# Kernel tuning notes

Hardware: AMD Instinct MI355X
Metric: run time of the kernel (lower is better)

The kernel has to match this reference:

```python
import jax, jax.numpy as jnp
import numpy as np

KS = 3          # kernel_size
NK = KS * KS    # sample points per output pixel
PAD = KS // 2   # 'same' zero padding


def setup_inputs() -> dict:
    key = jax.random.key(0)
    k1, k2, k3, k4 = jax.random.split(key, 4)
    B, H, W, C, F = 8, 64, 64, 128, 256
    x = jax.random.normal(k1, (B, H, W, C), jnp.float32)
    offset = jax.random.normal(k2, (B, H, W, 2 * NK), jnp.float32)
    modulation = jax.random.uniform(k3, (B, H, W, NK), jnp.float32)
    conv_kernel = jax.random.normal(k4, (KS, KS, C, F), jnp.float32) * 0.02
    conv_bias = jnp.zeros((F,), jnp.float32)
    return {"x": x, "offset": offset, "modulation": modulation,
            "conv_kernel": conv_kernel, "conv_bias": conv_bias}


def reference(x, offset, modulation, conv_kernel, conv_bias):
    B, H, W, C = x.shape
    # zero pad ('same')
    xp = jnp.pad(x, ((0, 0), (PAD, PAD), (PAD, PAD), (0, 0)))
    ih, iw = H + 2 * PAD, W + 2 * PAD

    # offset: first NK channels are y-offsets, last NK are x-offsets -> [B,H,W,NK,2]
    off = jnp.stack([offset[..., :NK], offset[..., NK:]], axis=-1)

    # pixel centers in padded coords (start at 1 due to padding), stride 1
    gy, gx = jnp.meshgrid(jnp.arange(1, H + 1), jnp.arange(1, W + 1), indexing="ij")
    pix = jnp.stack([gy, gx], -1).reshape(1, H, W, 1, 2).astype(x.dtype)

    # kernel tap offsets, ky varies slowest after flatten (matches TF source)
    ky, kx = jnp.meshgrid(jnp.arange(-PAD, KS - PAD), jnp.arange(-PAD, KS - PAD), indexing="ij")
    ker = jnp.stack([ky.reshape(-1), kx.reshape(-1)], -1).reshape(1, 1, 1, NK, 2).astype(x.dtype)

    p = off + pix + ker                       # [B,H,W,NK,2] sampling locations
    y0f = jnp.floor(p[..., 0])
    x0f = jnp.floor(p[..., 1])
    y0 = jnp.clip(y0f, 0, ih - 1)
    x0 = jnp.clip(x0f, 0, iw - 1)
    y1 = jnp.clip(y0f + 1.0, 0, ih - 1)
    x1 = jnp.clip(x0f + 1.0, 0, iw - 1)

    bidx = jnp.arange(B).reshape(B, 1, 1, 1)

    def gather(yi, xi):  # -> [B,H,W,NK,C]
        return xp[bidx, yi.astype(jnp.int32), xi.astype(jnp.int32)]

    f00 = gather(y0, x0)
    f01 = gather(y1, x0)
    f10 = gather(y0, x1)
    f11 = gather(y1, x1)

    py = jnp.clip(p[..., 0], 0, ih - 1)[..., None]
    px = jnp.clip(p[..., 1], 0, iw - 1)[..., None]
    ly = py - y0[..., None]
    lx = px - x0[..., None]

    feats = ((1.0 - ly) * (1.0 - lx) * f00 + (1.0 - ly) * lx * f01
             + ly * (1.0 - lx) * f10 + ly * lx * f11)      # [B,H,W,NK,C]
    feats = feats * modulation[..., None]

    # rearrange exactly as the TF code: concat kernel-row chunks along H, then reshape
    feats = jnp.concatenate([feats[:, :, :, s:s + KS, :] for s in range(0, NK, KS)], axis=1)
    feats = feats.reshape(B, H * KS, W * KS, C)

    out = jax.lax.conv_general_dilated(
        feats, conv_kernel, window_strides=(KS, KS), padding="VALID",
        dimension_numbers=("NHWC", "HWIO", "NHWC"))
    return out + conv_bias
```

## Files before the change

kernel.cpp:

```cpp
#include <hip/hip_runtime.h>

typedef __attribute__((ext_vector_type(8))) short short8;
typedef __attribute__((ext_vector_type(4))) float f32x4;

__device__ __forceinline__ unsigned short f2bf(float f) {
  union { float f; unsigned u; } v; v.f = f;
  unsigned r = v.u + 0x7FFFu + ((v.u >> 16) & 1u);
  return (unsigned short)(r >> 16);
}

__device__ __forceinline__ short8 pack8(f32x4 a, f32x4 b) {
  short8 p;
  p[0] = (short)f2bf(a.x); p[1] = (short)f2bf(a.y);
  p[2] = (short)f2bf(a.z); p[3] = (short)f2bf(a.w);
  p[4] = (short)f2bf(b.x); p[5] = (short)f2bf(b.y);
  p[6] = (short)f2bf(b.z); p[7] = (short)f2bf(b.w);
  return p;
}

__device__ __forceinline__ short8 packEO(f32x4 e, f32x4 o) {
  short8 p;
  p[0] = (short)f2bf(e.x); p[1] = (short)f2bf(o.x);
  p[2] = (short)f2bf(e.y); p[3] = (short)f2bf(o.y);
  p[4] = (short)f2bf(e.z); p[5] = (short)f2bf(o.z);
  p[6] = (short)f2bf(e.w); p[7] = (short)f2bf(o.w);
  return p;
}

constexpr int KKt = 1152;
constexpr int Ff  = 256;
constexpr size_t WT_BYTES = (size_t)KKt * Ff * 2;
constexpr size_t XB_BYTES = (size_t)8 * 64 * 64 * 128 * 2;

__global__ void wt_prep(const float* __restrict__ kf, unsigned short* __restrict__ wtB) {
  int idx = blockIdx.x * 256 + threadIdx.x;
  int j  = idx & 7;
  int fr = (idx >> 3) & 15;
  int kg = (idx >> 7) & 3;
  int ft = (idx >> 9) & 15;
  int ks = (idx >> 13) & 3;
  int ch = idx >> 15;
  int k = ch * 128 + ks * 32 + kg * 8 + j;
  int f = ft * 16 + fr;
  wtB[idx] = f2bf(kf[k * Ff + f]);
}

__global__ void x_prep(const float* __restrict__ x, unsigned short* __restrict__ xb) {
  int i = (blockIdx.x * 512 + threadIdx.x) * 8;
  const f32x4* p = (const f32x4*)(x + i);
  *(short8*)(xb + i) = pack8(p[0], p[1]);
}

__global__ __launch_bounds__(1024, 8) void dcn_bf16(
    const unsigned short* __restrict__ xb, const float* __restrict__ off,
    const float* __restrict__ mo, const unsigned short* __restrict__ wtB,
    const float* __restrict__ bias, float* __restrict__ out) {
  __shared__ __align__(16) char At[2][64 * 272];

  const int b  = blockIdx.x & 7;
  const int oh = blockIdx.x >> 3;
  const int t  = threadIdx.x;
  const int lane = t & 63;
  const int wv   = t >> 6;
  const int mh   = wv & 1;
  const int fq   = wv >> 1;
  const int fr   = lane & 15;
  const int kg   = lane >> 4;
  const int sow  = t >> 4;
  const int c8   = t & 15;

  f32x4 acc[2][2];
#pragma unroll
  for (int i = 0; i < 2; ++i) { acc[i][0] = f32x4{0,0,0,0}; acc[i][1] = f32x4{0,0,0,0}; }

  float oyr[2], oxr[2], mmr[2];
  int   og[4]; float wg[4];

  auto loadOff = [&](int ch, int sl) {
    const int dy = ch / 3, dxk = ch - dy * 3;
    const int r = 3 * oh + dy, hp = r & 63, kp = ((r >> 6) * 3) + dxk;
    const int pix = (b * 64 + hp) * 64 + sow;
    oyr[sl] = off[pix * 18 + kp];
    oxr[sl] = off[pix * 18 + 9 + kp];
    mmr[sl] = mo[pix * 9 + kp];
  };

  auto calcW = [&](int ch, int sl) {
    const int dy = ch / 3, dxk = ch - dy * 3;
    const int r = 3 * oh + dy, hp = r & 63, kp = ((r >> 6) * 3) + dxk;
    const float py = oyr[sl] + (float)(hp + kp / 3);
    const float px = oxr[sl] + (float)(sow + kp % 3);
    const float mm = mmr[sl];
    const float y0f = floorf(py), x0f = floorf(px);
    const float y0 = fminf(fmaxf(y0f, 0.f), 65.f);
    const float y1 = fminf(fmaxf(y0f + 1.f, 0.f), 65.f);
    const float x0 = fminf(fmaxf(x0f, 0.f), 65.f);
    const float x1 = fminf(fmaxf(x0f + 1.f, 0.f), 65.f);
    const float ly = fminf(fmaxf(py, 0.f), 65.f) - y0;
    const float lx = fminf(fmaxf(px, 0.f), 65.f) - x0;
    wg[0] = (1.f - ly) * (1.f - lx) * mm;
    wg[1] = (1.f - ly) * lx * mm;
    wg[2] = ly * (1.f - lx) * mm;
    wg[3] = ly * lx * mm;
    const int iy0 = (int)y0, iy1 = (int)y1, ix0 = (int)x0, ix1 = (int)x1;
    const int yy[4] = {iy0, iy1, iy0, iy1};
    const int xx[4] = {ix0, ix0, ix1, ix1};
#pragma unroll
    for (int j = 0; j < 4; ++j) {
      const bool v = (yy[j] >= 1) & (yy[j] <= 64) & (xx[j] >= 1) & (xx[j] <= 64);
      int o = ((b * 64 + yy[j] - 1) * 64 + (xx[j] - 1)) * 128 + c8 * 8;
      if (!v) { o = 0; wg[j] = 0.f; }
      og[j] = o;
    }
  };

  auto ldQ = [&](int c) -> short8 {
    return *(const short8*)(xb + og[c]);
  };
  auto accQ = [&](short8 s, float w, f32x4& Pe, f32x4& Po) {
    union { short8 s; unsigned u[4]; } v; v.s = s;
#pragma unroll
    for (int i = 0; i < 4; ++i) {
      union { unsigned u; float f; } e, o;
      e.u = v.u[i] << 16;
      o.u = v.u[i] & 0xffff0000u;
      Pe[i] = fmaf(w, e.f, Pe[i]);
      Po[i] = fmaf(w, o.f, Po[i]);
    }
  };

  auto mmah = [&](int buf, int ch, int ks) {
    const unsigned short* bp = wtB + (((ch * 4 + ks) * 16 + fq * 2) * 64 + lane) * 8;
    short8 bf0 = *(const short8*)bp;
    short8 bf1 = *(const short8*)(bp + 512);
    short8 af[2];
#pragma unroll
    for (int m2 = 0; m2 < 2; ++m2)
      af[m2] = *(const short8*)(At[buf] + (mh * 32 + m2 * 16 + fr) * 272 + ks * 64 + kg * 16);
#pragma unroll
    for (int m2 = 0; m2 < 2; ++m2) {
      acc[m2][0] = __builtin_amdgcn_mfma_f32_16x16x32_bf16(af[m2], bf0, acc[m2][0], 0, 0, 0);
      acc[m2][1] = __builtin_amdgcn_mfma_f32_16x16x32_bf16(af[m2], bf1, acc[m2][1], 0, 0, 0);
    }
  };

  const int wb = sow * 272 + c8 * 16;

  loadOff(0, 0); loadOff(1, 1);
  calcW(0, 0);
  {
    short8 q0 = ldQ(0), q1 = ldQ(1), q2 = ldQ(2), q3 = ldQ(3);
    f32x4 Pe{0,0,0,0}, Po{0,0,0,0};
    accQ(q0, wg[0], Pe, Po); accQ(q1, wg[1], Pe, Po);
    accQ(q2, wg[2], Pe, Po); accQ(q3, wg[3], Pe, Po);
    *(short8*)(At[0] + wb) = packEO(Pe, Po);
  }
  __syncthreads();

#pragma unroll
  for (int ch = 0; ch < 9; ++ch) {
    const int buf = ch & 1;
    const bool hv = ch < 8;
    short8 q0, q1, q2, q3;
    f32x4 Pe{0,0,0,0}, Po{0,0,0,0};
    if (hv) {
      calcW(ch + 1, (ch + 1) & 1);
      q0 = ldQ(0); q1 = ldQ(1);
    }
    mmah(buf, ch, 0);
    if (hv) {
      q2 = ldQ(2); q3 = ldQ(3);
      accQ(q0, wg[0], Pe, Po);
    }
    mmah(buf, ch, 1);
    if (hv) accQ(q1, wg[1], Pe, Po);
    if (ch < 7) loadOff(ch + 2, ch & 1);
    mmah(buf, ch, 2);
    if (hv) {
      accQ(q2, wg[2], Pe, Po);
      accQ(q3, wg[3], Pe, Po);
      *(short8*)(At[buf ^ 1] + wb) = packEO(Pe, Po);
    }
    mmah(buf, ch, 3);
    __syncthreads();
  }

  float bs[2];
#pragma unroll
  for (int nb = 0; nb < 2; ++nb) bs[nb] = bias[fq * 32 + nb * 16 + fr];
  float* orow = out + (long)(b * 64 + oh) * 64 * 256;
#pragma unroll
  for (int m2 = 0; m2 < 2; ++m2) {
#pragma unroll
    for (int j = 0; j < 4; ++j) {
      const int row = mh * 32 + m2 * 16 + kg * 4 + j;
#pragma unroll
      for (int nb = 0; nb < 2; ++nb)
        orow[row * 256 + fq * 32 + nb * 16 + fr] = acc[m2][nb][j] + bs[nb];
    }
  }
}

__global__ __launch_bounds__(512, 4) void dcn_f32(
    const float* __restrict__ x, const float* __restrict__ off,
    const float* __restrict__ mo, const unsigned short* __restrict__ wtB,
    const float* __restrict__ bias, float* __restrict__ out) {
  __shared__ __align__(16) char At[2][64 * 272];
  const int b  = blockIdx.x & 7;
  const int oh = blockIdx.x >> 3;
  const int t  = threadIdx.x;
  const int lane = t & 63;
  const int wv   = t >> 6;
  const int fr   = lane & 15;
  const int kg   = lane >> 4;
  const int sow  = t >> 3;
  const int c16  = t & 7;

  f32x4 acc[4][2];
#pragma unroll
  for (int i = 0; i < 4; ++i) { acc[i][0] = f32x4{0,0,0,0}; acc[i][1] = f32x4{0,0,0,0}; }
  float oyr[2], oxr[2], mmr[2];
  int   og[4]; float wg[4];

  auto loadOff = [&](int ch, int sl) {
    const int dy = ch / 3, dxk = ch - dy * 3;
    const int r = 3 * oh + dy, hp = r & 63, kp = ((r >> 6) * 3) + dxk;
    const int pix = (b * 64 + hp) * 64 + sow;
    oyr[sl] = off[pix * 18 + kp];
    oxr[sl] = off[pix * 18 + 9 + kp];
    mmr[sl] = mo[pix * 9 + kp];
  };
  auto calcW = [&](int ch, int sl) {
    const int dy = ch / 3, dxk = ch - dy * 3;
    const int r = 3 * oh + dy, hp = r & 63, kp = ((r >> 6) * 3) + dxk;
    const float py = oyr[sl] + (float)(hp + kp / 3);
    const float px = oxr[sl] + (float)(sow + kp % 3);
    const float mm = mmr[sl];
    const float y0f = floorf(py), x0f = floorf(px);
    const float y0 = fminf(fmaxf(y0f, 0.f), 65.f);
    const float y1 = fminf(fmaxf(y0f + 1.f, 0.f), 65.f);
    const float x0 = fminf(fmaxf(x0f, 0.f), 65.f);
    const float x1 = fminf(fmaxf(x0f + 1.f, 0.f), 65.f);
    const float ly = fminf(fmaxf(py, 0.f), 65.f) - y0;
    const float lx = fminf(fmaxf(px, 0.f), 65.f) - x0;
    wg[0] = (1.f - ly) * (1.f - lx) * mm;
    wg[1] = (1.f - ly) * lx * mm;
    wg[2] = ly * (1.f - lx) * mm;
    wg[3] = ly * lx * mm;
    const int iy0 = (int)y0, iy1 = (int)y1, ix0 = (int)x0, ix1 = (int)x1;
    const int yy[4] = {iy0, iy1, iy0, iy1};
    const int xx[4] = {ix0, ix0, ix1, ix1};
#pragma unroll
    for (int j = 0; j < 4; ++j) {
      const bool v = (yy[j] >= 1) & (yy[j] <= 64) & (xx[j] >= 1) & (xx[j] <= 64);
      int o = ((b * 64 + yy[j] - 1) * 64 + (xx[j] - 1)) * 128 + c16 * 16;
      if (!v) { o = 0; wg[j] = 0.f; }
      og[j] = o;
    }
  };
  auto ldB = [&](int ch, int ks, short8* bf) {
    const unsigned short* p = wtB + (((ch * 4 + ks) * 16 + wv * 2) * 64 + lane) * 8;
    bf[0] = *(const short8*)p;
    bf[1] = *(const short8*)(p + 512);
  };
  auto mmah = [&](int buf, int ks, const short8* bf) {
    short8 af[4];
#pragma unroll
    for (int m2 = 0; m2 < 4; ++m2)
      af[m2] = *(const short8*)(At[buf] + (m2 * 16 + fr) * 272 + ks * 64 + kg * 16);
#pragma unroll
    for (int m2 = 0; m2 < 4; ++m2)
#pragma unroll
      for (int nb = 0; nb < 2; ++nb)
        acc[m2][nb] = __builtin_amdgcn_mfma_f32_16x16x32_bf16(af[m2], bf[nb], acc[m2][nb], 0, 0, 0);
  };
  auto ldC = [&](int c, f32x4* G) {
    const f32x4* p = (const f32x4*)(x + og[c]);
    G[0] = p[0]; G[1] = p[1]; G[2] = p[2]; G[3] = p[3];
  };
  const int wb = sow * 272 + c16 * 32;
  loadOff(0, 0); loadOff(1, 1);
  calcW(0, 0);
  {
    f32x4 G0[4], G1[4];
    ldC(0, G0); ldC(1, G1);
    f32x4 P0 = wg[0]*G0[0] + wg[1]*G1[0], P1 = wg[0]*G0[1] + wg[1]*G1[1];
    f32x4 P2 = wg[0]*G0[2] + wg[1]*G1[2], P3 = wg[0]*G0[3] + wg[1]*G1[3];
    ldC(2, G0); ldC(3, G1);
    P0 += wg[2]*G0[0] + wg[3]*G1[0]; P1 += wg[2]*G0[1] + wg[3]*G1[1];
    P2 += wg[2]*G0[2] + wg[3]*G1[2]; P3 += wg[2]*G0[3] + wg[3]*G1[3];
    *(short8*)(At[0] + wb)      = pack8(P0, P1);
    *(short8*)(At[0] + wb + 16) = pack8(P2, P3);
  }
  __syncthreads();
#pragma unroll
  for (int ch = 0; ch < 9; ++ch) {
    const int buf = ch & 1;
    const bool hv = ch < 8;
    if (hv) calcW(ch + 1, (ch + 1) & 1);
    short8 bA[2], bB[2];
    f32x4 G0[4], G1[4], P0, P1, P2, P3;
    ldB(ch, 0, bA);
    if (hv) ldC(0, G0);
    ldB(ch, 1, bB);
    mmah(buf, 0, bA);
    if (hv) { P0 = wg[0]*G0[0]; P1 = wg[0]*G0[1]; P2 = wg[0]*G0[2]; P3 = wg[0]*G0[3]; }
    if (hv) ldC(1, G1);
    ldB(ch, 2, bA);
    mmah(buf, 1, bB);
    if (hv) { P0 += wg[1]*G1[0]; P1 += wg[1]*G1[1]; P2 += wg[1]*G1[2]; P3 += wg[1]*G1[3]; }
    if (hv) ldC(2, G0);
    ldB(ch, 3, bB);
    if (ch < 7) loadOff(ch + 2, ch & 1);
    mmah(buf, 2, bA);
    if (hv) { P0 += wg[2]*G0[0]; P1 += wg[2]*G0[1]; P2 += wg[2]*G0[2]; P3 += wg[2]*G0[3]; }
    if (hv) ldC(3, G1);
    mmah(buf, 3, bB);
    if (hv) {
      P0 += wg[3]*G1[0]; P1 += wg[3]*G1[1]; P2 += wg[3]*G1[2]; P3 += wg[3]*G1[3];
      *(short8*)(At[buf ^ 1] + wb)      = pack8(P0, P1);
      *(short8*)(At[buf ^ 1] + wb + 16) = pack8(P2, P3);
    }
    __syncthreads();
  }
  float bs[2];
#pragma unroll
  for (int nb = 0; nb < 2; ++nb) bs[nb] = bias[wv * 32 + nb * 16 + fr];
  float* orow = out + (long)(b * 64 + oh) * 64 * 256;
#pragma unroll
  for (int m2 = 0; m2 < 4; ++m2) {
#pragma unroll
    for (int j = 0; j < 4; ++j) {
      const int ow = m2 * 16 + kg * 4 + j;
#pragma unroll
      for (int nb = 0; nb < 2; ++nb)
        orow[ow * 256 + wv * 32 + nb * 16 + fr] = acc[m2][nb][j] + bs[nb];
    }
  }
}

extern "C" void kernel_launch(void* const* d_in, const int* in_sizes, int n_in,
                              void* d_out, int out_size, void* d_ws, size_t ws_size,
                              hipStream_t stream) {
  const float* x    = (const float*)d_in[0];
  const float* off  = (const float*)d_in[1];
  const float* mo   = (const float*)d_in[2];
  const float* kf   = (const float*)d_in[3];
  const float* bias = (const float*)d_in[4];
  float* outp = (float*)d_out;
  unsigned short* wtB = (unsigned short*)d_ws;

  wt_prep<<<1152, 256, 0, stream>>>(kf, wtB);
  if (ws_size >= WT_BYTES + XB_BYTES) {
    unsigned short* xb = (unsigned short*)((char*)d_ws + WT_BYTES);
    x_prep<<<1024, 512, 0, stream>>>(x, xb);
    dcn_bf16<<<512, 1024, 0, stream>>>(xb, off, mo, wtB, bias, outp);
  } else {
    dcn_f32<<<512, 512, 0, stream>>>(x, off, mo, wtB, bias, outp);
  }
}
```

Baseline: 57.05 us.

## Precompute bilinear sample records in a fused prep kernel and simplify main loop

```diff
diff --git a/kernel.cpp b/kernel.cpp
--- a/kernel.cpp
+++ b/kernel.cpp
@@ -2,6 +2,7 @@
 
 typedef __attribute__((ext_vector_type(8))) short short8;
 typedef __attribute__((ext_vector_type(4))) float f32x4;
+typedef __attribute__((ext_vector_type(4))) int   int4v;
 
 __device__ __forceinline__ unsigned short f2bf(float f) {
   union { float f; unsigned u; } v; v.f = f;
@@ -29,8 +30,190 @@
 
 constexpr int KKt = 1152;
 constexpr int Ff  = 256;
-constexpr size_t WT_BYTES = (size_t)KKt * Ff * 2;
-constexpr size_t XB_BYTES = (size_t)8 * 64 * 64 * 128 * 2;
+constexpr size_t WT_BYTES  = (size_t)KKt * Ff * 2;
+constexpr size_t XB_BYTES  = (size_t)8 * 64 * 64 * 128 * 2;
+constexpr size_t REC_BYTES = (size_t)8 * 192 * 3 * 64 * 32;
+
+__global__ __launch_bounds__(256) void prep_all(
+    const float* __restrict__ x, const float* __restrict__ off,
+    const float* __restrict__ mo, const float* __restrict__ kf,
+    unsigned short* __restrict__ wtB, unsigned short* __restrict__ xb,
+    float* __restrict__ rec) {
+  const int bid = blockIdx.x;
+  if (bid < 2048) {
+    int i = (bid * 256 + threadIdx.x) * 8;
+    const f32x4* p = (const f32x4*)(x + i);
+    *(short8*)(xb + i) = pack8(p[0], p[1]);
+  } else if (bid < 2048 + 1152) {
+    int idx = (bid - 2048) * 256 + threadIdx.x;
+    int j  = idx & 7;
+    int fr = (idx >> 3) & 15;
+    int kg = (idx >> 7) & 3;
+    int ft = (idx >> 9) & 15;
+    int ks = (idx >> 13) & 3;
+    int ch = idx >> 15;
+    int k = ch * 128 + ks * 32 + kg * 8 + j;
+    int f = ft * 16 + fr;
+    wtB[idx] = f2bf(kf[k * Ff + f]);
+  } else {
+    int s  = (bid - 3200) * 256 + threadIdx.x;
+    int w  = s & 63;
+    int t1 = s >> 6;
+    int dxk = t1 % 3;
+    int t2  = t1 / 3;
+    int r   = t2 % 192;
+    int b   = t2 / 192;
+    int hp  = r & 63;
+    int kp  = (r >> 6) * 3 + dxk;
+    int pix = (b * 64 + hp) * 64 + w;
+    float oy = off[pix * 18 + kp];
+    float ox = off[pix * 18 + 9 + kp];
+    float mm = mo[pix * 9 + kp];
+    float py = oy + (float)(hp + kp / 3);
+    float px = ox + (float)(w + kp % 3);
+    float y0f = floorf(py), x0f = floorf(px);
+    float y0 = fminf(fmaxf(y0f, 0.f), 65.f);
+    float y1 = fminf(fmaxf(y0f + 1.f, 0.f), 65.f);
+    float x0 = fminf(fmaxf(x0f, 0.f), 65.f);
+    float x1 = fminf(fmaxf(x0f + 1.f, 0.f), 65.f);
+    float ly = fminf(fmaxf(py, 0.f), 65.f) - y0;
+    float lx = fminf(fmaxf(px, 0.f), 65.f) - x0;
+    f32x4 wv;
+    wv.x = (1.f - ly) * (1.f - lx) * mm;
+    wv.y = (1.f - ly) * lx * mm;
+    wv.z = ly * (1.f - lx) * mm;
+    wv.w = ly * lx * mm;
+    const int iy0 = (int)y0, iy1 = (int)y1, ix0 = (int)x0, ix1 = (int)x1;
+    const int yy[4] = {iy0, iy1, iy0, iy1};
+    const int xx[4] = {ix0, ix0, ix1, ix1};
+    int4v ov;
+#pragma unroll
+    for (int j2 = 0; j2 < 4; ++j2) {
+      const bool v = (yy[j2] >= 1) & (yy[j2] <= 64) & (xx[j2] >= 1) & (xx[j2] <= 64);
+      int o = ((b * 64 + yy[j2] - 1) * 64 + (xx[j2] - 1)) * 128;
+      if (!v) { o = 0; wv[j2] = 0.f; }
+      ov[j2] = o;
+    }
+    ((f32x4*)rec)[s * 2]     = wv;
+    ((int4v*)rec)[s * 2 + 1] = ov;
+  }
+}
+
+__global__ __launch_bounds__(1024, 8) void dcn_rec(
+    const unsigned short* __restrict__ xb, const unsigned short* __restrict__ wtB,
+    const float* __restrict__ rec, const float* __restrict__ bias,
+    float* __restrict__ out) {
+  __shared__ __align__(16) char At[2][64 * 272];
+
+  const int b  = blockIdx.x & 7;
+  const int oh = blockIdx.x >> 3;
+  const int t  = threadIdx.x;
+  const int lane = t & 63;
+  const int wv   = t >> 6;
+  const int mh   = wv & 1;
+  const int fq   = wv >> 1;
+  const int fr   = lane & 15;
+  const int kg   = lane >> 4;
+  const int sow  = t >> 4;
+  const int c8   = t & 15;
+
+  f32x4 acc[2][2];
+#pragma unroll
+  for (int i = 0; i < 2; ++i) { acc[i][0] = f32x4{0,0,0,0}; acc[i][1] = f32x4{0,0,0,0}; }
+
+  const f32x4* rp = (const f32x4*)rec + (size_t)((b * 576 + 9 * oh) * 64) * 2;
+
+  auto ldR = [&](int ch, f32x4& w4, int4v& o4) {
+    const f32x4* p = rp + (ch * 64 + sow) * 2;
+    w4 = p[0];
+    o4 = *(const int4v*)(p + 1);
+  };
+  auto issueG = [&](int4v o4, short8* q) {
+    q[0] = *(const short8*)(xb + o4.x + c8 * 8);
+    q[1] = *(const short8*)(xb + o4.y + c8 * 8);
+    q[2] = *(const short8*)(xb + o4.z + c8 * 8);
+    q[3] = *(const short8*)(xb + o4.w + c8 * 8);
+  };
+  auto accQ = [&](short8 s, float w, f32x4& Pe, f32x4& Po) {
+    union { short8 s; unsigned u[4]; } v; v.s = s;
+#pragma unroll
+    for (int i = 0; i < 4; ++i) {
+      union { unsigned u; float f; } e, o;
+      e.u = v.u[i] << 16;
+      o.u = v.u[i] & 0xffff0000u;
+      Pe[i] = fmaf(w, e.f, Pe[i]);
+      Po[i] = fmaf(w, o.f, Po[i]);
+    }
+  };
+  auto combine = [&](const short8* q, f32x4 w4) -> short8 {
+    f32x4 Pe{0,0,0,0}, Po{0,0,0,0};
+    accQ(q[0], w4.x, Pe, Po);
+    accQ(q[1], w4.y, Pe, Po);
+    accQ(q[2], w4.z, Pe, Po);
+    accQ(q[3], w4.w, Pe, Po);
+    return packEO(Pe, Po);
+  };
+  auto mmah = [&](int buf, int ch, int ks) {
+    const unsigned short* bp = wtB + (((ch * 4 + ks) * 16 + fq * 2) * 64 + lane) * 8;
+    short8 bf0 = *(const short8*)bp;
+    short8 bf1 = *(const short8*)(bp + 512);
+    short8 af[2];
+#pragma unroll
+    for (int m2 = 0; m2 < 2; ++m2)
+      af[m2] = *(const short8*)(At[buf] + (mh * 32 + m2 * 16 + fr) * 272 + ks * 64 + kg * 16);
+#pragma unroll
+    for (int m2 = 0; m2 < 2; ++m2) {
+      acc[m2][0] = __builtin_amdgcn_mfma_f32_16x16x32_bf16(af[m2], bf0, acc[m2][0], 0, 0, 0);
+      acc[m2][1] = __builtin_amdgcn_mfma_f32_16x16x32_bf16(af[m2], bf1, acc[m2][1], 0, 0, 0);
+    }
+  };
+
+  const int wb = sow * 272 + c8 * 16;
+
+  short8 q[4];
+  f32x4  w4s[2];
+  int4v  o4;
+
+  ldR(0, w4s[0], o4);
+  issueG(o4, q);
+  {
+    int4v o4b;
+    ldR(1, w4s[1], o4b);
+    *(short8*)(At[0] + wb) = combine(q, w4s[0]);
+    issueG(o4b, q);
+  }
+  __syncthreads();
+
+#pragma unroll
+  for (int ch = 0; ch < 9; ++ch) {
+    const int buf = ch & 1;
+    int4v o4n;
+    if (ch < 7) ldR(ch + 2, w4s[ch & 1], o4n);
+    if (ch < 8)
+      *(short8*)(At[buf ^ 1] + wb) = combine(q, w4s[(ch + 1) & 1]);
+    mmah(buf, ch, 0);
+    mmah(buf, ch, 1);
+    if (ch < 7) issueG(o4n, q);
+    mmah(buf, ch, 2);
+    mmah(buf, ch, 3);
+    __syncthreads();
+  }
+
+  float bs[2];
+#pragma unroll
+  for (int nb = 0; nb < 2; ++nb) bs[nb] = bias[fq * 32 + nb * 16 + fr];
+  float* orow = out + (long)(b * 64 + oh) * 64 * 256;
+#pragma unroll
+  for (int m2 = 0; m2 < 2; ++m2) {
+#pragma unroll
+    for (int j = 0; j < 4; ++j) {
+      const int row = mh * 32 + m2 * 16 + kg * 4 + j;
+#pragma unroll
+      for (int nb = 0; nb < 2; ++nb)
+        orow[row * 256 + fq * 32 + nb * 16 + fr] = acc[m2][nb][j] + bs[nb];
+    }
+  }
+}
 
 __global__ void wt_prep(const float* __restrict__ kf, unsigned short* __restrict__ wtB) {
   int idx = blockIdx.x * 256 + threadIdx.x;
@@ -56,7 +239,6 @@
     const float* __restrict__ mo, const unsigned short* __restrict__ wtB,
     const float* __restrict__ bias, float* __restrict__ out) {
   __shared__ __align__(16) char At[2][64 * 272];
-
   const int b  = blockIdx.x & 7;
   const int oh = blockIdx.x >> 3;
   const int t  = threadIdx.x;
@@ -72,7 +254,6 @@
   f32x4 acc[2][2];
 #pragma unroll
   for (int i = 0; i < 2; ++i) { acc[i][0] = f32x4{0,0,0,0}; acc[i][1] = f32x4{0,0,0,0}; }
-
   float oyr[2], oxr[2], mmr[2];
   int   og[4]; float wg[4];
 
@@ -84,7 +265,6 @@
     oxr[sl] = off[pix * 18 + 9 + kp];
     mmr[sl] = mo[pix * 9 + kp];
   };
-
   auto calcW = [&](int ch, int sl) {
     const int dy = ch / 3, dxk = ch - dy * 3;
     const int r = 3 * oh + dy, hp = r & 63, kp = ((r >> 6) * 3) + dxk;
@@ -113,10 +293,7 @@
       og[j] = o;
     }
   };
-
-  auto ldQ = [&](int c) -> short8 {
-    return *(const short8*)(xb + og[c]);
-  };
+  auto ldQ = [&](int c) -> short8 { return *(const short8*)(xb + og[c]); };
   auto accQ = [&](short8 s, float w, f32x4& Pe, f32x4& Po) {
     union { short8 s; unsigned u[4]; } v; v.s = s;
 #pragma unroll
@@ -128,7 +305,6 @@
       Po[i] = fmaf(w, o.f, Po[i]);
     }
   };
-
   auto mmah = [&](int buf, int ch, int ks) {
     const unsigned short* bp = wtB + (((ch * 4 + ks) * 16 + fq * 2) * 64 + lane) * 8;
     short8 bf0 = *(const short8*)bp;
@@ -143,9 +319,7 @@
       acc[m2][1] = __builtin_amdgcn_mfma_f32_16x16x32_bf16(af[m2], bf1, acc[m2][1], 0, 0, 0);
     }
   };
-
   const int wb = sow * 272 + c8 * 16;
-
   loadOff(0, 0); loadOff(1, 1);
   calcW(0, 0);
   {
@@ -156,7 +330,6 @@
     *(short8*)(At[0] + wb) = packEO(Pe, Po);
   }
   __syncthreads();
-
 #pragma unroll
   for (int ch = 0; ch < 9; ++ch) {
     const int buf = ch & 1;
@@ -184,7 +357,6 @@
     mmah(buf, ch, 3);
     __syncthreads();
   }
-
   float bs[2];
 #pragma unroll
   for (int nb = 0; nb < 2; ++nb) bs[nb] = bias[fq * 32 + nb * 16 + fr];
@@ -197,144 +369,6 @@
 #pragma unroll
       for (int nb = 0; nb < 2; ++nb)
         orow[row * 256 + fq * 32 + nb * 16 + fr] = acc[m2][nb][j] + bs[nb];
-    }
-  }
-}
-
-__global__ __launch_bounds__(512, 4) void dcn_f32(
-    const float* __restrict__ x, const float* __restrict__ off,
-    const float* __restrict__ mo, const unsigned short* __restrict__ wtB,
-    const float* __restrict__ bias, float* __restrict__ out) {
-  __shared__ __align__(16) char At[2][64 * 272];
-  const int b  = blockIdx.x & 7;
-  const int oh = blockIdx.x >> 3;
-  const int t  = threadIdx.x;
-  const int lane = t & 63;
-  const int wv   = t >> 6;
-  const int fr   = lane & 15;
-  const int kg   = lane >> 4;
-  const int sow  = t >> 3;
-  const int c16  = t & 7;
-
-  f32x4 acc[4][2];
-#pragma unroll
-  for (int i = 0; i < 4; ++i) { acc[i][0] = f32x4{0,0,0,0}; acc[i][1] = f32x4{0,0,0,0}; }
-  float oyr[2], oxr[2], mmr[2];
-  int   og[4]; float wg[4];
-
-  auto loadOff = [&](int ch, int sl) {
-    const int dy = ch / 3, dxk = ch - dy * 3;
-    const int r = 3 * oh + dy, hp = r & 63, kp = ((r >> 6) * 3) + dxk;
-    const int pix = (b * 64 + hp) * 64 + sow;
-    oyr[sl] = off[pix * 18 + kp];
-    oxr[sl] = off[pix * 18 + 9 + kp];
-    mmr[sl] = mo[pix * 9 + kp];
-  };
-  auto calcW = [&](int ch, int sl) {
-    const int dy = ch / 3, dxk = ch - dy * 3;
-    const int r = 3 * oh + dy, hp = r & 63, kp = ((r >> 6) * 3) + dxk;
-    const float py = oyr[sl] + (float)(hp + kp / 3);
-    const float px = oxr[sl] + (float)(sow + kp % 3);
-    const float mm = mmr[sl];
-    const float y0f = floorf(py), x0f = floorf(px);
-    const float y0 = fminf(fmaxf(y0f, 0.f), 65.f);
-    const float y1 = fminf(fmaxf(y0f + 1.f, 0.f), 65.f);
-    const float x0 = fminf(fmaxf(x0f, 0.f), 65.f);
-    const float x1 = fminf(fmaxf(x0f + 1.f, 0.f), 65.f);
-    const float ly = fminf(fmaxf(py, 0.f), 65.f) - y0;
-    const float lx = fminf(fmaxf(px, 0.f), 65.f) - x0;
-    wg[0] = (1.f - ly) * (1.f - lx) * mm;
-    wg[1] = (1.f - ly) * lx * mm;
-    wg[2] = ly * (1.f - lx) * mm;
-    wg[3] = ly * lx * mm;
-    const int iy0 = (int)y0, iy1 = (int)y1, ix0 = (int)x0, ix1 = (int)x1;
-    const int yy[4] = {iy0, iy1, iy0, iy1};
-    const int xx[4] = {ix0, ix0, ix1, ix1};
-#pragma unroll
-    for (int j = 0; j < 4; ++j) {
-      const bool v = (yy[j] >= 1) & (yy[j] <= 64) & (xx[j] >= 1) & (xx[j] <= 64);
-      int o = ((b * 64 + yy[j] - 1) * 64 + (xx[j] - 1)) * 128 + c16 * 16;
-      if (!v) { o = 0; wg[j] = 0.f; }
-      og[j] = o;
-    }
-  };
-  auto ldB = [&](int ch, int ks, short8* bf) {
-    const unsigned short* p = wtB + (((ch * 4 + ks) * 16 + wv * 2) * 64 + lane) * 8;
-    bf[0] = *(const short8*)p;
-    bf[1] = *(const short8*)(p + 512);
-  };
-  auto mmah = [&](int buf, int ks, const short8* bf) {
-    short8 af[4];
-#pragma unroll
-    for (int m2 = 0; m2 < 4; ++m2)
-      af[m2] = *(const short8*)(At[buf] + (m2 * 16 + fr) * 272 + ks * 64 + kg * 16);
-#pragma unroll
-    for (int m2 = 0; m2 < 4; ++m2)
-#pragma unroll
-      for (int nb = 0; nb < 2; ++nb)
-        acc[m2][nb] = __builtin_amdgcn_mfma_f32_16x16x32_bf16(af[m2], bf[nb], acc[m2][nb], 0, 0, 0);
-  };
-  auto ldC = [&](int c, f32x4* G) {
-    const f32x4* p = (const f32x4*)(x + og[c]);
-    G[0] = p[0]; G[1] = p[1]; G[2] = p[2]; G[3] = p[3];
-  };
-  const int wb = sow * 272 + c16 * 32;
-  loadOff(0, 0); loadOff(1, 1);
-  calcW(0, 0);
-  {
-    f32x4 G0[4], G1[4];
-    ldC(0, G0); ldC(1, G1);
-    f32x4 P0 = wg[0]*G0[0] + wg[1]*G1[0], P1 = wg[0]*G0[1] + wg[1]*G1[1];
-    f32x4 P2 = wg[0]*G0[2] + wg[1]*G1[2], P3 = wg[0]*G0[3] + wg[1]*G1[3];
-    ldC(2, G0); ldC(3, G1);
-    P0 += wg[2]*G0[0] + wg[3]*G1[0]; P1 += wg[2]*G0[1] + wg[3]*G1[1];
-    P2 += wg[2]*G0[2] + wg[3]*G1[2]; P3 += wg[2]*G0[3] + wg[3]*G1[3];
-    *(short8*)(At[0] + wb)      = pack8(P0, P1);
-    *(short8*)(At[0] + wb + 16) = pack8(P2, P3);
-  }
-  __syncthreads();
-#pragma unroll
-  for (int ch = 0; ch < 9; ++ch) {
-    const int buf = ch & 1;
-    const bool hv = ch < 8;
-    if (hv) calcW(ch + 1, (ch + 1) & 1);
-    short8 bA[2], bB[2];
-    f32x4 G0[4], G1[4], P0, P1, P2, P3;
-    ldB(ch, 0, bA);
-    if (hv) ldC(0, G0);
-    ldB(ch, 1, bB);
-    mmah(buf, 0, bA);
-    if (hv) { P0 = wg[0]*G0[0]; P1 = wg[0]*G0[1]; P2 = wg[0]*G0[2]; P3 = wg[0]*G0[3]; }
-    if (hv) ldC(1, G1);
-    ldB(ch, 2, bA);
-    mmah(buf, 1, bB);
-    if (hv) { P0 += wg[1]*G1[0]; P1 += wg[1]*G1[1]; P2 += wg[1]*G1[2]; P3 += wg[1]*G1[3]; }
-    if (hv) ldC(2, G0);
-    ldB(ch, 3, bB);
-    if (ch < 7) loadOff(ch + 2, ch & 1);
-    mmah(buf, 2, bA);
-    if (hv) { P0 += wg[2]*G0[0]; P1 += wg[2]*G0[1]; P2 += wg[2]*G0[2]; P3 += wg[2]*G0[3]; }
-    if (hv) ldC(3, G1);
-    mmah(buf, 3, bB);
-    if (hv) {
-      P0 += wg[3]*G1[0]; P1 += wg[3]*G1[1]; P2 += wg[3]*G1[2]; P3 += wg[3]*G1[3];
-      *(short8*)(At[buf ^ 1] + wb)      = pack8(P0, P1);
-      *(short8*)(At[buf ^ 1] + wb + 16) = pack8(P2, P3);
-    }
-    __syncthreads();
-  }
-  float bs[2];
-#pragma unroll
-  for (int nb = 0; nb < 2; ++nb) bs[nb] = bias[wv * 32 + nb * 16 + fr];
-  float* orow = out + (long)(b * 64 + oh) * 64 * 256;
-#pragma unroll
-  for (int m2 = 0; m2 < 4; ++m2) {
-#pragma unroll
-    for (int j = 0; j < 4; ++j) {
-      const int ow = m2 * 16 + kg * 4 + j;
-#pragma unroll
-      for (int nb = 0; nb < 2; ++nb)
-        orow[ow * 256 + wv * 32 + nb * 16 + fr] = acc[m2][nb][j] + bs[nb];
     }
   }
 }
@@ -349,13 +383,15 @@
   const float* bias = (const float*)d_in[4];
   float* outp = (float*)d_out;
   unsigned short* wtB = (unsigned short*)d_ws;
-
-  wt_prep<<<1152, 256, 0, stream>>>(kf, wtB);
-  if (ws_size >= WT_BYTES + XB_BYTES) {
-    unsigned short* xb = (unsigned short*)((char*)d_ws + WT_BYTES);
+  unsigned short* xb  = (unsigned short*)((char*)d_ws + WT_BYTES);
+
+  if (ws_size >= WT_BYTES + XB_BYTES + REC_BYTES) {
+    float* rec = (float*)((char*)d_ws + WT_BYTES + XB_BYTES);
+    prep_all<<<4352, 256, 0, stream>>>(x, off, mo, kf, wtB, xb, rec);
+    dcn_rec<<<512, 1024, 0, stream>>>(xb, wtB, rec, bias, outp);
+  } else {
+    wt_prep<<<1152, 256, 0, stream>>>(kf, wtB);
     x_prep<<<1024, 512, 0, stream>>>(x, xb);
     dcn_bf16<<<512, 1024, 0, stream>>>(xb, off, mo, wtB, bias, outp);
-  } else {
-    dcn_f32<<<512, 512, 0, stream>>>(x, off, mo, wtB, bias, outp);
-  }
-}
+  }
+}
```

Result: slower. 63.12 us (+10.6%).

## Split deformable sampling into a separate bf16 im2col pass and a pipelined GEMM

Applied to the files above, without the earlier changes.

```diff
diff --git a/kernel.cpp b/kernel.cpp
--- a/kernel.cpp
+++ b/kernel.cpp
@@ -31,24 +31,178 @@
 constexpr int Ff  = 256;
 constexpr size_t WT_BYTES = (size_t)KKt * Ff * 2;
 constexpr size_t XB_BYTES = (size_t)8 * 64 * 64 * 128 * 2;
-
-__global__ void wt_prep(const float* __restrict__ kf, unsigned short* __restrict__ wtB) {
-  int idx = blockIdx.x * 256 + threadIdx.x;
-  int j  = idx & 7;
-  int fr = (idx >> 3) & 15;
-  int kg = (idx >> 7) & 3;
-  int ft = (idx >> 9) & 15;
-  int ks = (idx >> 13) & 3;
-  int ch = idx >> 15;
-  int k = ch * 128 + ks * 32 + kg * 8 + j;
-  int f = ft * 16 + fr;
-  wtB[idx] = f2bf(kf[k * Ff + f]);
-}
-
-__global__ void x_prep(const float* __restrict__ x, unsigned short* __restrict__ xb) {
-  int i = (blockIdx.x * 512 + threadIdx.x) * 8;
-  const f32x4* p = (const f32x4*)(x + i);
-  *(short8*)(xb + i) = pack8(p[0], p[1]);
+constexpr size_t FE_BYTES = (size_t)32768 * KKt * 2;
+
+#define GLOAD_LDS16(g, l)                                          \
+  __builtin_amdgcn_global_load_lds(                                \
+      (const __attribute__((address_space(1))) void*)(g),          \
+      (__attribute__((address_space(3))) void*)(l), 16, 0, 0)
+
+__global__ __launch_bounds__(256) void prep_small(
+    const float* __restrict__ x, const float* __restrict__ kf,
+    unsigned short* __restrict__ xb, unsigned short* __restrict__ wtB) {
+  const int bid = blockIdx.x;
+  if (bid < 2048) {
+    int i = (bid * 256 + threadIdx.x) * 8;
+    const f32x4* p = (const f32x4*)(x + i);
+    *(short8*)(xb + i) = pack8(p[0], p[1]);
+  } else {
+    int idx = (bid - 2048) * 256 + threadIdx.x;
+    int j  = idx & 7;
+    int fr = (idx >> 3) & 15;
+    int kg = (idx >> 7) & 3;
+    int ft = (idx >> 9) & 15;
+    int ks = (idx >> 13) & 3;
+    int ch = idx >> 15;
+    int k = ch * 128 + ks * 32 + kg * 8 + j;
+    int f = ft * 16 + fr;
+    wtB[idx] = f2bf(kf[k * Ff + f]);
+  }
+}
+
+__global__ __launch_bounds__(1024, 8) void feats_prep(
+    const unsigned short* __restrict__ xb, const float* __restrict__ off,
+    const float* __restrict__ mo, char* __restrict__ feats) {
+  const int b  = blockIdx.x & 7;
+  const int oh = blockIdx.x >> 3;
+  const int t  = threadIdx.x;
+  const int sow = t >> 4;
+  const int c8  = t & 15;
+  const int r   = ((oh & 1) << 6) | sow;
+  const int mt  = (b << 5) | (oh >> 1);
+  const int swz = ((c8 & 7) << 4) ^ ((sow & 7) << 4);
+
+  for (int ch = 0; ch < 9; ++ch) {
+    const int dy = ch / 3, dxk = ch - dy * 3;
+    const int rr = 3 * oh + dy, hp = rr & 63, kp = ((rr >> 6) * 3) + dxk;
+    const int pix = (b * 64 + hp) * 64 + sow;
+    const float oy = off[pix * 18 + kp];
+    const float ox = off[pix * 18 + 9 + kp];
+    const float mm = mo[pix * 9 + kp];
+    const float py = oy + (float)(hp + kp / 3);
+    const float px = ox + (float)(sow + kp % 3);
+    const float y0f = floorf(py), x0f = floorf(px);
+    const float y0 = fminf(fmaxf(y0f, 0.f), 65.f);
+    const float y1 = fminf(fmaxf(y0f + 1.f, 0.f), 65.f);
+    const float x0 = fminf(fmaxf(x0f, 0.f), 65.f);
+    const float x1 = fminf(fmaxf(x0f + 1.f, 0.f), 65.f);
+    const float ly = fminf(fmaxf(py, 0.f), 65.f) - y0;
+    const float lx = fminf(fmaxf(px, 0.f), 65.f) - x0;
+    float wg[4];
+    wg[0] = (1.f - ly) * (1.f - lx) * mm;
+    wg[1] = (1.f - ly) * lx * mm;
+    wg[2] = ly * (1.f - lx) * mm;
+    wg[3] = ly * lx * mm;
+    const int iy0 = (int)y0, iy1 = (int)y1, ix0 = (int)x0, ix1 = (int)x1;
+    const int yy[4] = {iy0, iy1, iy0, iy1};
+    const int xx[4] = {ix0, ix0, ix1, ix1};
+    int og[4];
+#pragma unroll
+    for (int j = 0; j < 4; ++j) {
+      const bool v = (yy[j] >= 1) & (yy[j] <= 64) & (xx[j] >= 1) & (xx[j] <= 64);
+      int o = ((b * 64 + yy[j] - 1) * 64 + (xx[j] - 1)) * 128 + c8 * 8;
+      if (!v) { o = 0; wg[j] = 0.f; }
+      og[j] = o;
+    }
+    short8 q0 = *(const short8*)(xb + og[0]);
+    short8 q1 = *(const short8*)(xb + og[1]);
+    short8 q2 = *(const short8*)(xb + og[2]);
+    short8 q3 = *(const short8*)(xb + og[3]);
+    f32x4 Pe{0, 0, 0, 0}, Po{0, 0, 0, 0};
+    auto accQ = [&](short8 s, float w) {
+      union { short8 s; unsigned u[4]; } v; v.s = s;
+#pragma unroll
+      for (int i = 0; i < 4; ++i) {
+        union { unsigned u; float f; } e, o;
+        e.u = v.u[i] << 16;
+        o.u = v.u[i] & 0xffff0000u;
+        Pe[i] = fmaf(w, e.f, Pe[i]);
+        Po[i] = fmaf(w, o.f, Po[i]);
+      }
+    };
+    accQ(q0, wg[0]); accQ(q1, wg[1]); accQ(q2, wg[2]); accQ(q3, wg[3]);
+    const int kstep = ch * 2 + (c8 >> 3);
+    const size_t dst = ((size_t)(kstep * 256 + mt) << 14) + (size_t)r * 128 + swz;
+    *(short8*)(feats + dst) = packEO(Pe, Po);
+  }
+}
+
+__global__ __launch_bounds__(512, 4) void dcn_gemm(
+    const char* __restrict__ feats, const unsigned short* __restrict__ wtB,
+    const float* __restrict__ bias, float* __restrict__ out) {
+  __shared__ __align__(16) char As[2][16384];
+
+  const int bid = blockIdx.x;
+  const int b   = bid & 7;
+  const int q   = bid >> 3;
+  const int nt  = q & 1;
+  const int mt  = (b << 5) | (q >> 1);
+  const int t   = threadIdx.x;
+  const int lane = t & 63;
+  const int wv   = t >> 6;
+  const int wc   = wv & 3;
+  const int wr   = wv >> 2;
+  const int fr   = lane & 15;
+  const int kg   = lane >> 4;
+
+  f32x4 acc[4][2];
+#pragma unroll
+  for (int i = 0; i < 4; ++i) { acc[i][0] = f32x4{0,0,0,0}; acc[i][1] = f32x4{0,0,0,0}; }
+
+  const char* Abase = feats + ((size_t)mt << 14);
+  const int loff = (wv << 11) + (lane << 4);
+
+  auto stage = [&](int buf, int ks) {
+    const char* g = Abase + ((size_t)ks << 22);
+    GLOAD_LDS16(g + loff,        &As[buf][wv << 11]);
+    GLOAD_LDS16(g + loff + 1024, &As[buf][(wv << 11) + 1024]);
+  };
+
+  auto compute = [&](int buf, int ks) {
+#pragma unroll
+    for (int ks2 = 0; ks2 < 2; ++ks2) {
+      short8 af[4];
+#pragma unroll
+      for (int m2 = 0; m2 < 4; ++m2) {
+        const int rr = wr * 64 + m2 * 16 + fr;
+        af[m2] = *(const short8*)&As[buf][rr * 128 + ((ks2 * 64 + kg * 16) ^ ((rr & 7) << 4))];
+      }
+      const int ch = ks >> 1, ksB = ((ks & 1) << 1) | ks2;
+      const unsigned short* bp =
+          wtB + ((((ch * 4 + ksB) * 16 + nt * 8 + wc * 2) * 64 + lane) << 3);
+      short8 bf0 = *(const short8*)bp;
+      short8 bf1 = *(const short8*)(bp + 512);
+#pragma unroll
+      for (int m2 = 0; m2 < 4; ++m2) {
+        acc[m2][0] = __builtin_amdgcn_mfma_f32_16x16x32_bf16(af[m2], bf0, acc[m2][0], 0, 0, 0);
+        acc[m2][1] = __builtin_amdgcn_mfma_f32_16x16x32_bf16(af[m2], bf1, acc[m2][1], 0, 0, 0);
+      }
+    }
+  };
+
+  stage(0, 0);
+  __syncthreads();
+#pragma unroll 2
+  for (int ks = 0; ks < 18; ++ks) {
+    const int buf = ks & 1;
+    if (ks < 17) stage(buf ^ 1, ks + 1);
+    compute(buf, ks);
+    __syncthreads();
+  }
+
+  const int n0 = nt * 128 + wc * 32;
+  const float bs0 = bias[n0 + fr];
+  const float bs1 = bias[n0 + 16 + fr];
+  float* obase = out + (size_t)(mt * 128 + wr * 64) * 256 + n0;
+#pragma unroll
+  for (int m2 = 0; m2 < 4; ++m2) {
+#pragma unroll
+    for (int j = 0; j < 4; ++j) {
+      float* orow = obase + (size_t)(m2 * 16 + kg * 4 + j) * 256;
+      orow[fr]      = acc[m2][0][j] + bs0;
+      orow[16 + fr] = acc[m2][1][j] + bs1;
+    }
+  }
 }
 
 __global__ __launch_bounds__(1024, 8) void dcn_bf16(
@@ -56,7 +210,6 @@
     const float* __restrict__ mo, const unsigned short* __restrict__ wtB,
     const float* __restrict__ bias, float* __restrict__ out) {
   __shared__ __align__(16) char At[2][64 * 272];
-
   const int b  = blockIdx.x & 7;
   const int oh = blockIdx.x >> 3;
   const int t  = threadIdx.x;
@@ -72,7 +225,6 @@
   f32x4 acc[2][2];
 #pragma unroll
   for (int i = 0; i < 2; ++i) { acc[i][0] = f32x4{0,0,0,0}; acc[i][1] = f32x4{0,0,0,0}; }
-
   float oyr[2], oxr[2], mmr[2];
   int   og[4]; float wg[4];
 
@@ -84,7 +236,6 @@
     oxr[sl] = off[pix * 18 + 9 + kp];
     mmr[sl] = mo[pix * 9 + kp];
   };
-
   auto calcW = [&](int ch, int sl) {
     const int dy = ch / 3, dxk = ch - dy * 3;
     const int r = 3 * oh + dy, hp = r & 63, kp = ((r >> 6) * 3) + dxk;
@@ -113,10 +264,7 @@
       og[j] = o;
     }
   };
-
-  auto ldQ = [&](int c) -> short8 {
-    return *(const short8*)(xb + og[c]);
-  };
+  auto ldQ = [&](int c) -> short8 { return *(const short8*)(xb + og[c]); };
   auto accQ = [&](short8 s, float w, f32x4& Pe, f32x4& Po) {
     union { short8 s; unsigned u[4]; } v; v.s = s;
 #pragma unroll
@@ -128,7 +276,6 @@
       Po[i] = fmaf(w, o.f, Po[i]);
     }
   };
-
   auto mmah = [&](int buf, int ch, int ks) {
     const unsigned short* bp = wtB + (((ch * 4 + ks) * 16 + fq * 2) * 64 + lane) * 8;
     short8 bf0 = *(const short8*)bp;
@@ -143,9 +290,7 @@
       acc[m2][1] = __builtin_amdgcn_mfma_f32_16x16x32_bf16(af[m2], bf1, acc[m2][1], 0, 0, 0);
     }
   };
-
   const int wb = sow * 272 + c8 * 16;
-
   loadOff(0, 0); loadOff(1, 1);
   calcW(0, 0);
   {
@@ -156,7 +301,6 @@
     *(short8*)(At[0] + wb) = packEO(Pe, Po);
   }
   __syncthreads();
-
 #pragma unroll
   for (int ch = 0; ch < 9; ++ch) {
     const int buf = ch & 1;
@@ -184,7 +328,6 @@
     mmah(buf, ch, 3);
     __syncthreads();
   }
-
   float bs[2];
 #pragma unroll
   for (int nb = 0; nb < 2; ++nb) bs[nb] = bias[fq * 32 + nb * 16 + fr];
@@ -197,144 +340,6 @@
 #pragma unroll
       for (int nb = 0; nb < 2; ++nb)
         orow[row * 256 + fq * 32 + nb * 16 + fr] = acc[m2][nb][j] + bs[nb];
-    }
-  }
-}
-
-__global__ __launch_bounds__(512, 4) void dcn_f32(
-    const float* __restrict__ x, const float* __restrict__ off,
-    const float* __restrict__ mo, const unsigned short* __restrict__ wtB,
-    const float* __restrict__ bias, float* __restrict__ out) {
-  __shared__ __align__(16) char At[2][64 * 272];
-  const int b  = blockIdx.x & 7;
-  const int oh = blockIdx.x >> 3;
-  const int t  = threadIdx.x;
-  const int lane = t & 63;
-  const int wv   = t >> 6;
-  const int fr   = lane & 15;
-  const int kg   = lane >> 4;
-  const int sow  = t >> 3;
-  const int c16  = t & 7;
-
-  f32x4 acc[4][2];
-#pragma unroll
-  for (int i = 0; i < 4; ++i) { acc[i][0] = f32x4{0,0,0,0}; acc[i][1] = f32x4{0,0,0,0}; }
-  float oyr[2], oxr[2], mmr[2];
-  int   og[4]; float wg[4];
-
-  auto loadOff = [&](int ch, int sl) {
-    const int dy = ch / 3, dxk = ch - dy * 3;
-    const int r = 3 * oh + dy, hp = r & 63, kp = ((r >> 6) * 3) + dxk;
-    const int pix = (b * 64 + hp) * 64 + sow;
-    oyr[sl] = off[pix * 18 + kp];
-    oxr[sl] = off[pix * 18 + 9 + kp];
-    mmr[sl] = mo[pix * 9 + kp];
-  };
-  auto calcW = [&](int ch, int sl) {
-    const int dy = ch / 3, dxk = ch - dy * 3;
-    const int r = 3 * oh + dy, hp = r & 63, kp = ((r >> 6) * 3) + dxk;
-    const float py = oyr[sl] + (float)(hp + kp / 3);
-    const float px = oxr[sl] + (float)(sow + kp % 3);
-    const float mm = mmr[sl];
-    const float y0f = floorf(py), x0f = floorf(px);
-    const float y0 = fminf(fmaxf(y0f, 0.f), 65.f);
-    const float y1 = fminf(fmaxf(y0f + 1.f, 0.f), 65.f);
-    const float x0 = fminf(fmaxf(x0f, 0.f), 65.f);
-    const float x1 = fminf(fmaxf(x0f + 1.f, 0.f), 65.f);
-    const float ly = fminf(fmaxf(py, 0.f), 65.f) - y0;
-    const float lx = fminf(fmaxf(px, 0.f), 65.f) - x0;
-    wg[0] = (1.f - ly) * (1.f - lx) * mm;
-    wg[1] = (1.f - ly) * lx * mm;
-    wg[2] = ly * (1.f - lx) * mm;
-    wg[3] = ly * lx * mm;
-    const int iy0 = (int)y0, iy1 = (int)y1, ix0 = (int)x0, ix1 = (int)x1;
-    const int yy[4] = {iy0, iy1, iy0, iy1};
-    const int xx[4] = {ix0, ix0, ix1, ix1};
-#pragma unroll
-    for (int j = 0; j < 4; ++j) {
-      const bool v = (yy[j] >= 1) & (yy[j] <= 64) & (xx[j] >= 1) & (xx[j] <= 64);
-      int o = ((b * 64 + yy[j] - 1) * 64 + (xx[j] - 1)) * 128 + c16 * 16;
-      if (!v) { o = 0; wg[j] = 0.f; }
-      og[j] = o;
-    }
-  };
-  auto ldB = [&](int ch, int ks, short8* bf) {
-    const unsigned short* p = wtB + (((ch * 4 + ks) * 16 + wv * 2) * 64 + lane) * 8;
-    bf[0] = *(const short8*)p;
-    bf[1] = *(const short8*)(p + 512);
-  };
-  auto mmah = [&](int buf, int ks, const short8* bf) {
-    short8 af[4];
-#pragma unroll
-    for (int m2 = 0; m2 < 4; ++m2)
-      af[m2] = *(const short8*)(At[buf] + (m2 * 16 + fr) * 272 + ks * 64 + kg * 16);
-#pragma unroll
-    for (int m2 = 0; m2 < 4; ++m2)
-#pragma unroll
-      for (int nb = 0; nb < 2; ++nb)
-        acc[m2][nb] = __builtin_amdgcn_mfma_f32_16x16x32_bf16(af[m2], bf[nb], acc[m2][nb], 0, 0, 0);
-  };
-  auto ldC = [&](int c, f32x4* G) {
-    const f32x4* p = (const f32x4*)(x + og[c]);
-    G[0] = p[0]; G[1] = p[1]; G[2] = p[2]; G[3] = p[3];
-  };
-  const int wb = sow * 272 + c16 * 32;
-  loadOff(0, 0); loadOff(1, 1);
-  calcW(0, 0);
-  {
-    f32x4 G0[4], G1[4];
-    ldC(0, G0); ldC(1, G1);
-    f32x4 P0 = wg[0]*G0[0] + wg[1]*G1[0], P1 = wg[0]*G0[1] + wg[1]*G1[1];
-    f32x4 P2 = wg[0]*G0[2] + wg[1]*G1[2], P3 = wg[0]*G0[3] + wg[1]*G1[3];
-    ldC(2, G0); ldC(3, G1);
-    P0 += wg[2]*G0[0] + wg[3]*G1[0]; P1 += wg[2]*G0[1] + wg[3]*G1[1];
-    P2 += wg[2]*G0[2] + wg[3]*G1[2]; P3 += wg[2]*G0[3] + wg[3]*G1[3];
-    *(short8*)(At[0] + wb)      = pack8(P0, P1);
-    *(short8*)(At[0] + wb + 16) = pack8(P2, P3);
-  }
-  __syncthreads();
-#pragma unroll
-  for (int ch = 0; ch < 9; ++ch) {
-    const int buf = ch & 1;
-    const bool hv = ch < 8;
-    if (hv) calcW(ch + 1, (ch + 1) & 1);
-    short8 bA[2], bB[2];
-    f32x4 G0[4], G1[4], P0, P1, P2, P3;
-    ldB(ch, 0, bA);
-    if (hv) ldC(0, G0);
-    ldB(ch, 1, bB);
-    mmah(buf, 0, bA);
-    if (hv) { P0 = wg[0]*G0[0]; P1 = wg[0]*G0[1]; P2 = wg[0]*G0[2]; P3 = wg[0]*G0[3]; }
-    if (hv) ldC(1, G1);
-    ldB(ch, 2, bA);
-    mmah(buf, 1, bB);
-    if (hv) { P0 += wg[1]*G1[0]; P1 += wg[1]*G1[1]; P2 += wg[1]*G1[2]; P3 += wg[1]*G1[3]; }
-    if (hv) ldC(2, G0);
-    ldB(ch, 3, bB);
-    if (ch < 7) loadOff(ch + 2, ch & 1);
-    mmah(buf, 2, bA);
-    if (hv) { P0 += wg[2]*G0[0]; P1 += wg[2]*G0[1]; P2 += wg[2]*G0[2]; P3 += wg[2]*G0[3]; }
-    if (hv) ldC(3, G1);
-    mmah(buf, 3, bB);
-    if (hv) {
-      P0 += wg[3]*G1[0]; P1 += wg[3]*G1[1]; P2 += wg[3]*G1[2]; P3 += wg[3]*G1[3];
-      *(short8*)(At[buf ^ 1] + wb)      = pack8(P0, P1);
-      *(short8*)(At[buf ^ 1] + wb + 16) = pack8(P2, P3);
-    }
-    __syncthreads();
-  }
-  float bs[2];
-#pragma unroll
-  for (int nb = 0; nb < 2; ++nb) bs[nb] = bias[wv * 32 + nb * 16 + fr];
-  float* orow = out + (long)(b * 64 + oh) * 64 * 256;
-#pragma unroll
-  for (int m2 = 0; m2 < 4; ++m2) {
-#pragma unroll
-    for (int j = 0; j < 4; ++j) {
-      const int ow = m2 * 16 + kg * 4 + j;
-#pragma unroll
-      for (int nb = 0; nb < 2; ++nb)
-        orow[ow * 256 + wv * 32 + nb * 16 + fr] = acc[m2][nb][j] + bs[nb];
     }
   }
 }
@@ -349,13 +354,14 @@
   const float* bias = (const float*)d_in[4];
   float* outp = (float*)d_out;
   unsigned short* wtB = (unsigned short*)d_ws;
-
-  wt_prep<<<1152, 256, 0, stream>>>(kf, wtB);
-  if (ws_size >= WT_BYTES + XB_BYTES) {
-    unsigned short* xb = (unsigned short*)((char*)d_ws + WT_BYTES);
-    x_prep<<<1024, 512, 0, stream>>>(x, xb);
+  unsigned short* xb  = (unsigned short*)((char*)d_ws + WT_BYTES);
+
+  prep_small<<<3200, 256, 0, stream>>>(x, kf, xb, wtB);
+  if (ws_size >= WT_BYTES + XB_BYTES + FE_BYTES) {
+    char* feats = (char*)d_ws + WT_BYTES + XB_BYTES;
+    feats_prep<<<512, 1024, 0, stream>>>(xb, off, mo, feats);
+    dcn_gemm<<<512, 512, 0, stream>>>(feats, wtB, bias, outp);
+  } else {
     dcn_bf16<<<512, 1024, 0, stream>>>(xb, off, mo, wtB, bias, outp);
-  } else {
-    dcn_f32<<<512, 512, 0, stream>>>(x, off, mo, wtB, bias, outp);
-  }
-}
+  }
+}
```

After: 60.07 us. +5.3%, slower.
